# Kernel tuning notes

Measured on AMD Instinct MI355X. Metric: run time of the kernel, lower is better.

## Reference

```python
import jax, jax.numpy as jnp
import numpy as np

N = 100000   # nodes
E = 600000   # edges (before self loops)
D = 128      # dim_latent = H*F
H = 4        # heads
F = 32       # out_feats per head
L = 3        # num GATConv layers (conv_0 + 2)


def setup_inputs() -> dict:
    key = jax.random.key(0)
    ks = jax.random.split(key, 10)
    return {
        "weights": jax.random.normal(ks[0], (N,), jnp.float32),
        "lin_W": jax.random.normal(ks[1], (D, 1), jnp.float32) * 0.1,
        "lin_b": jnp.zeros((D,), jnp.float32),
        "fc_W": jax.random.normal(ks[2], (L, D, D), jnp.float32) * (1.0 / np.sqrt(D)),
        "attn_l": jax.random.normal(ks[3], (L, H, F), jnp.float32) * 0.1,
        "attn_r": jax.random.normal(ks[4], (L, H, F), jnp.float32) * 0.1,
        "conv_b": jnp.zeros((L, D), jnp.float32),
        "pred_W": jax.random.normal(ks[5], (1, D), jnp.float32) * 0.1,
        "pred_b": jnp.zeros((1,), jnp.float32),
        "src": jax.random.randint(ks[6], (E,), 0, N, jnp.int32),
        "dst": jax.random.randint(ks[7], (E,), 0, N, jnp.int32),
    }


def _leaky(x, slope):
    return jnp.where(x >= 0, x, slope * x)


def _gat_conv(x, fc_W, attn_l, attn_r, bias, src, dst):
    # DGL GATConv: bias-free fc, per-head additive attention, edge softmax over dst
    h = (x @ fc_W.T).reshape(N, H, F)                      # [N,H,F]
    el = jnp.sum(h * attn_l[None], axis=-1)                # [N,H]
    er = jnp.sum(h * attn_r[None], axis=-1)                # [N,H]
    e = _leaky(el[src] + er[dst], 0.2)                     # [Etot,H]
    m = jax.ops.segment_max(e, dst, num_segments=N)        # [N,H]
    a = jnp.exp(e - m[dst])                                # [Etot,H]
    s = jax.ops.segment_sum(a, dst, num_segments=N)        # [N,H]
    alpha = a / s[dst]                                     # [Etot,H]
    msg = h[src] * alpha[:, :, None]                       # [Etot,H,F]
    out = jax.ops.segment_sum(msg, dst, num_segments=N)    # [N,H,F]
    out = out + bias.reshape(H, F)[None]
    return out.reshape(N, H * F)


def reference(weights, lin_W, lin_b, fc_W, attn_l, attn_r, conv_b, pred_W, pred_b, src, dst):
    # add self loops (dgl.add_self_loop)
    loop = jnp.arange(N, dtype=src.dtype)
    s_full = jnp.concatenate([src, loop])
    d_full = jnp.concatenate([dst, loop])

    x = weights[:, None] @ lin_W.T + lin_b                 # [N,D]
    for i in range(L):
        if i > 0:
            x = _leaky(x, 0.01)                            # nn.LeakyReLU default
        x = _gat_conv(x, fc_W[i], attn_l[i], attn_r[i], conv_b[i], s_full, d_full)
    logits = x @ pred_W.T + pred_b                         # [N,1]
    return logits
```

## Files before the change

### kernel.cpp

```cpp
#include <hip/hip_runtime.h>
#include <hip/hip_bf16.h>
#include <math.h>


__device__ __forceinline__ float leaky02(float x) {
    return x >= 0.f ? x : 0.2f * x;
}
__device__ __forceinline__ float leaky01(float x) {
    return x >= 0.f ? x : 0.01f * x;
}

__device__ __forceinline__ unsigned short f2bf(float f) {
    unsigned u = __float_as_uint(f);
    unsigned r = u + 0x7FFFu + ((u >> 16) & 1u);
    return (unsigned short)(r >> 16);
}
__device__ __forceinline__ float bf2f(unsigned short s) {
    return __uint_as_float(((unsigned)s) << 16);
}

typedef __attribute__((ext_vector_type(8))) short bf16x8;
typedef __attribute__((ext_vector_type(8))) unsigned short u16x8;
typedef __attribute__((ext_vector_type(4))) float f32x4;

__global__ __launch_bounds__(1024) void prep_kernel(
    int* __restrict__ deg, int N,
    const float* __restrict__ fc_W, const float* __restrict__ attn_l,
    const float* __restrict__ attn_r,
    short* __restrict__ Wh, short* __restrict__ Wl,
    short* __restrict__ Mh, short* __restrict__ Ml,
    const float* __restrict__ lW, const float* __restrict__ lb,
    const float* __restrict__ cb2, const float* __restrict__ pW,
    const float* __restrict__ pb,
    float* __restrict__ c1, float* __restrict__ c2, float* __restrict__ prm,
    int* __restrict__ base_ctr)
{
    const int nbi = (N + 1023) >> 10;
    const int b = blockIdx.x;
    const int t = threadIdx.x;
    if (b == 0 && t == 0) *base_ctr = 0;

    if (b < nbi) {
        int i = b * 1024 + t;
        if (i < N) deg[i] = 1;
        if (i < 2 * 16384) {
            const float* W = fc_W + 16384;
            int l    = i >> 14;
            int p    = i & 16383;
            int j    = p & 7;
            int lane = (p >> 3) & 63;
            int c    = (p >> 9) & 7;
            int kk   = p >> 12;
            int mr   = lane & 15;
            int quad = lane >> 4;
            int row  = c * 16 + mr;
            int d    = kk * 32 + quad * 8 + j;
            float f = W[(size_t)l * 16384 + row * 128 + d];
            unsigned short hi = f2bf(f);
            Wh[i] = (short)hi;
            Wl[i] = (short)f2bf(f - bf2f(hi));
        }
    } else if (b < nbi + 2) {
        int l = b - nbi;
        const float* W  = fc_W + (size_t)(l + 1) * 16384;
        const float* al = attn_l + (l + 1) * 128;
        const float* ar = attn_r + (l + 1) * 128;
        short* mh = Mh + (size_t)l * 16 * 128;
        short* ml = Ml + (size_t)l * 16 * 128;
        int r = t >> 7;
        int d = t & 127;
        int hh = r & 3;
        const float* av = (r < 4) ? al : ar;
        float s = 0.f;
#pragma unroll
        for (int f = 0; f < 32; ++f)
            s += W[(size_t)(hh * 32 + f) * 128 + d] * av[hh * 32 + f];
        unsigned short hi = f2bf(s);
        mh[r * 128 + d] = (short)hi;
        ml[r * 128 + d] = (short)f2bf(s - bf2f(hi));
        mh[(r + 8) * 128 + d] = 0;
        ml[(r + 8) * 128 + d] = 0;
    } else {
        __shared__ float sh1[128], sh2[128], sh3[128], sh4[128], sh5[128];
        const float* W0 = fc_W;
        const float* al = attn_l;
        const float* ar = attn_r;
        int j = t >> 3, sub = t & 7;
        float s1 = 0.f, s2 = 0.f;
        int d0 = sub * 16;
#pragma unroll
        for (int k = 0; k < 16; ++k) {
            float wv = W0[j * 128 + d0 + k];
            s1 += lW[d0 + k] * wv;
            s2 += lb[d0 + k] * wv;
        }
#pragma unroll
        for (int m = 1; m <= 4; m <<= 1) {
            s1 += __shfl_xor(s1, m, 64);
            s2 += __shfl_xor(s2, m, 64);
        }
        if (sub == 0) {
            c1[j] = s1; c2[j] = s2;
            sh1[j] = s1 * al[j]; sh2[j] = s2 * al[j];
            sh3[j] = s1 * ar[j]; sh4[j] = s2 * ar[j];
            sh5[j] = cb2[j] * pW[j];
        }
        __syncthreads();
        if (t < 4) {
            float p = 0.f, q = 0.f, r = 0.f, s = 0.f;
            for (int f = 0; f < 32; ++f) {
                p += sh1[t * 32 + f]; q += sh2[t * 32 + f];
                r += sh3[t * 32 + f]; s += sh4[t * 32 + f];
            }
            prm[t] = p; prm[4 + t] = q; prm[8 + t] = r; prm[12 + t] = s;
        }
        if (t == 0) {
            float cs = 0.f;
            for (int k = 0; k < 128; ++k) cs += sh5[k];
            prm[16] = cs + pb[0];
        }
    }
}

__global__ __launch_bounds__(256) void deg_count_slot_kernel(
    const int* __restrict__ dst, int* __restrict__ deg,
    int* __restrict__ slot, int E)
{
    int i = blockIdx.x * 256 + threadIdx.x;
    if (i < E) slot[i] = atomicAdd(&deg[dst[i]], 1);
}

__global__ __launch_bounds__(1024) void scan_kernel(
    const int* __restrict__ deg, int* __restrict__ base_ctr,
    int* __restrict__ rowp, int* __restrict__ col, int N)
{
    __shared__ int sh[1024];
    __shared__ int sbase;
    int b = blockIdx.x, t = threadIdx.x;
    int i = b * 1024 + t;
    int v = (i < N) ? deg[i] : 0;
    sh[t] = v;
    __syncthreads();
    for (int off = 1; off < 1024; off <<= 1) {
        int u = (t >= off) ? sh[t - off] : 0;
        __syncthreads();
        sh[t] += u;
        __syncthreads();
    }
    if (t == 1023) sbase = atomicAdd(base_ctr, sh[1023]);
    __syncthreads();
    int pre = sbase + sh[t] - v;
    if (i < N) {
        rowp[i] = pre;
        col[pre] = i;
    }
}

__global__ __launch_bounds__(256) void scatter2_kernel(
    const int* __restrict__ src, const int* __restrict__ dst,
    const int* __restrict__ slot, const int* __restrict__ rowp,
    int* __restrict__ col, int E)
{
    int i = blockIdx.x * 256 + threadIdx.x;
    if (i < E) col[rowp[dst[i]] + slot[i]] = src[i];
}

__global__ __launch_bounds__(256) void agg0_kernel(
    const float* __restrict__ w, const float* __restrict__ c1,
    const float* __restrict__ c2, const float* __restrict__ prm,
    const int* __restrict__ rowp, const int* __restrict__ deg,
    const int* __restrict__ col, const float* __restrict__ bias,
    unsigned short* __restrict__ xout, int N)
{
    const int lane = threadIdx.x & 63;
    const int q    = lane >> 4;
    const int l16  = lane & 15;
    const int v    = blockIdx.x * 16 + (threadIdx.x >> 6) * 4 + q;
    if (v >= N) return;

    const int r0 = rowp[v];
    const int r1 = r0 + deg[v];
    const int head = l16 >> 2;
    const int e4   = l16 & 3;
    const int f0   = l16 * 8;
    const float pl = prm[head],     ql = prm[4 + head];
    const float pr = prm[8 + head], qr = prm[12 + head];

    const float wv  = w[v];
    const float erq = wv * pr + qr;
    const float mref = leaky02(wv * pl + ql + erq);

    float S = 0.f, Sw = 0.f;
    for (int j = r0 + e4; j < r1; j += 4) {
        int u = col[j];
        float wu = w[u];
        float e = leaky02(wu * pl + ql + erq);
        float d = fminf(e - mref, 80.f);
        float p = __expf(d);
        S += p; Sw += p * wu;
    }
    S  += __shfl_xor(S, 1, 64);  S  += __shfl_xor(S, 2, 64);
    Sw += __shfl_xor(Sw, 1, 64); Sw += __shfl_xor(Sw, 2, 64);
    const float t = Sw / S;

    float4 a0 = *reinterpret_cast<const float4*>(&c1[f0]);
    float4 a1 = *reinterpret_cast<const float4*>(&c1[f0 + 4]);
    float4 g0 = *reinterpret_cast<const float4*>(&c2[f0]);
    float4 g1 = *reinterpret_cast<const float4*>(&c2[f0 + 4]);
    float4 b0 = *reinterpret_cast<const float4*>(&bias[f0]);
    float4 b1 = *reinterpret_cast<const float4*>(&bias[f0 + 4]);
    const float aa[8] = {a0.x, a0.y, a0.z, a0.w, a1.x, a1.y, a1.z, a1.w};
    const float gg[8] = {g0.x, g0.y, g0.z, g0.w, g1.x, g1.y, g1.z, g1.w};
    const float bb[8] = {b0.x, b0.y, b0.z, b0.w, b1.x, b1.y, b1.z, b1.w};

    u16x8 o;
#pragma unroll
    for (int k = 0; k < 8; ++k)
        o[k] = f2bf(leaky01(t * aa[k] + gg[k] + bb[k]));
    *reinterpret_cast<u16x8*>(&xout[(size_t)v * 128 + f0]) = o;
}

__global__ __launch_bounds__(256) void gemm_mfma_kernel(
    const unsigned short* __restrict__ xb, const short* __restrict__ Wh,
    const short* __restrict__ Wl, const short* __restrict__ Mh,
    const short* __restrict__ Ml, unsigned short* __restrict__ hb,
    float* __restrict__ el, float* __restrict__ er,
    const float* __restrict__ pW, float* __restrict__ yel,
    int N, int mode)
{
    const int lane = threadIdx.x & 63;
    const int wv   = threadIdx.x >> 6;
    const int m0   = blockIdx.x * 128 + wv * 32;
    const int mr   = lane & 15;
    const int quad = lane >> 4;

    int r0 = m0 + mr;      if (r0 > N - 1) r0 = N - 1;
    int r1 = m0 + 16 + mr; if (r1 > N - 1) r1 = N - 1;
    const unsigned short* xp0 = xb + (size_t)r0 * 128 + quad * 8;
    const unsigned short* xp1 = xb + (size_t)r1 * 128 + quad * 8;

    f32x4 acc0[8], acc1[8], acce0, acce1;
#pragma unroll
    for (int c = 0; c < 8; ++c) {
        acc0[c] = (f32x4){0.f, 0.f, 0.f, 0.f};
        acc1[c] = (f32x4){0.f, 0.f, 0.f, 0.f};
    }
    acce0 = (f32x4){0.f, 0.f, 0.f, 0.f};
    acce1 = (f32x4){0.f, 0.f, 0.f, 0.f};

#pragma unroll
    for (int kk = 0; kk < 4; ++kk) {
        bf16x8 a0 = *reinterpret_cast<const bf16x8*>(xp0 + kk * 32);
        bf16x8 a1 = *reinterpret_cast<const bf16x8*>(xp1 + kk * 32);

        const int kb = kk * 32 + quad * 8;
        bf16x8 bh[8], bl[8];
#pragma unroll
        for (int c = 0; c < 8; ++c) {
            const size_t wo = (size_t)((kk * 8 + c) * 64 + lane) * 8;
            bh[c] = *reinterpret_cast<const bf16x8*>(Wh + wo);
            bl[c] = *reinterpret_cast<const bf16x8*>(Wl + wo);
        }
        bf16x8 eh = *reinterpret_cast<const bf16x8*>(Mh + (size_t)mr * 128 + kb);
        bf16x8 eo = *reinterpret_cast<const bf16x8*>(Ml + (size_t)mr * 128 + kb);
#pragma unroll
        for (int c = 0; c < 8; ++c) {
            acc0[c] = __builtin_amdgcn_mfma_f32_16x16x32_bf16(a0, bh[c], acc0[c], 0, 0, 0);
            acc0[c] = __builtin_amdgcn_mfma_f32_16x16x32_bf16(a0, bl[c], acc0[c], 0, 0, 0);
            acc1[c] = __builtin_amdgcn_mfma_f32_16x16x32_bf16(a1, bh[c], acc1[c], 0, 0, 0);
            acc1[c] = __builtin_amdgcn_mfma_f32_16x16x32_bf16(a1, bl[c], acc1[c], 0, 0, 0);
        }
        acce0 = __builtin_amdgcn_mfma_f32_16x16x32_bf16(a0, eh, acce0, 0, 0, 0);
        acce0 = __builtin_amdgcn_mfma_f32_16x16x32_bf16(a0, eo, acce0, 0, 0, 0);
        acce1 = __builtin_amdgcn_mfma_f32_16x16x32_bf16(a1, eh, acce1, 0, 0, 0);
        acce1 = __builtin_amdgcn_mfma_f32_16x16x32_bf16(a1, eo, acce1, 0, 0, 0);
    }

    if (mode == 0) {
#pragma unroll
        for (int i = 0; i < 4; ++i) {
            int rowA = m0 + quad * 4 + i;
            if (rowA < N) {
                unsigned short* hp = hb + (size_t)rowA * 128 + mr;
#pragma unroll
                for (int c = 0; c < 8; ++c) hp[c * 16] = f2bf(acc0[c][i]);
                if (mr < 4)       el[(size_t)rowA * 4 + mr]       = acce0[i];
                else if (mr < 8)  er[(size_t)rowA * 4 + (mr - 4)] = acce0[i];
            }
            int rowB = m0 + 16 + quad * 4 + i;
            if (rowB < N) {
                unsigned short* hp = hb + (size_t)rowB * 128 + mr;
#pragma unroll
                for (int c = 0; c < 8; ++c) hp[c * 16] = f2bf(acc1[c][i]);
                if (mr < 4)       el[(size_t)rowB * 4 + mr]       = acce1[i];
                else if (mr < 8)  er[(size_t)rowB * 4 + (mr - 4)] = acce1[i];
            }
        }
    } else {
        float pw[8];
#pragma unroll
        for (int c = 0; c < 8; ++c) pw[c] = pW[mr + c * 16];
#pragma unroll
        for (int i = 0; i < 4; ++i) {
            int rowA = m0 + quad * 4 + i;
            {
                float y[4];
#pragma unroll
                for (int h = 0; h < 4; ++h)
                    y[h] = acc0[2 * h][i] * pw[2 * h] + acc0[2 * h + 1][i] * pw[2 * h + 1];
#pragma unroll
                for (int d = 1; d < 16; d <<= 1) {
#pragma unroll
                    for (int h = 0; h < 4; ++h) y[h] += __shfl_xor(y[h], d, 64);
                }
                if (rowA < N) {
                    if (mr < 4) {
                        float2 o; o.x = y[mr]; o.y = acce0[i];
                        *reinterpret_cast<float2*>(&yel[(size_t)rowA * 8 + mr * 2]) = o;
                    } else if (mr < 8) {
                        er[(size_t)rowA * 4 + (mr - 4)] = acce0[i];
                    }
                }
            }
            int rowB = m0 + 16 + quad * 4 + i;
            {
                float y[4];
#pragma unroll
                for (int h = 0; h < 4; ++h)
                    y[h] = acc1[2 * h][i] * pw[2 * h] + acc1[2 * h + 1][i] * pw[2 * h + 1];
#pragma unroll
                for (int d = 1; d < 16; d <<= 1) {
#pragma unroll
                    for (int h = 0; h < 4; ++h) y[h] += __shfl_xor(y[h], d, 64);
                }
                if (rowB < N) {
                    if (mr < 4) {
                        float2 o; o.x = y[mr]; o.y = acce1[i];
                        *reinterpret_cast<float2*>(&yel[(size_t)rowB * 8 + mr * 2]) = o;
                    } else if (mr < 8) {
                        er[(size_t)rowB * 4 + (mr - 4)] = acce1[i];
                    }
                }
            }
        }
    }
}

__global__ __launch_bounds__(256) void agg_mid_kernel(
    const unsigned short* __restrict__ hb, const float* __restrict__ el,
    const float* __restrict__ er, const int* __restrict__ rowp,
    const int* __restrict__ deg, const int* __restrict__ col,
    const float* __restrict__ bias, unsigned short* __restrict__ xout, int N)
{
    const int lane = threadIdx.x & 63;
    const int q    = lane >> 4;
    const int l16  = lane & 15;
    const int v    = blockIdx.x * 16 + (threadIdx.x >> 6) * 4 + q;
    if (v >= N) return;

    const int r0 = rowp[v];
    const int r1 = r0 + deg[v];
    const int head = l16 >> 2;
    const int f0   = l16 * 8;
    const float erq = er[(size_t)v * 4 + head];
    const float el_self = el[(size_t)v * 4 + head];
    const float mref = leaky02(el_self + erq);

    float s = 0.f;
    float acc[8];
#pragma unroll
    for (int k = 0; k < 8; ++k) acc[k] = 0.f;

    float elA = el_self;
    u16x8 hvA = *reinterpret_cast<const u16x8*>(&hb[(size_t)v * 128 + f0]);
    int jB = (r0 + 1 < r1) ? r0 + 1 : r1 - 1;
    int uB = col[jB];
    float elB = el[(size_t)uB * 4 + head];
    u16x8 hvB = *reinterpret_cast<const u16x8*>(&hb[(size_t)uB * 128 + f0]);

    for (int j = r0; j < r1; j += 2) {
        int jA2 = (j + 2 < r1) ? j + 2 : r1 - 1;
        int uA2 = col[jA2];
        float elA2 = el[(size_t)uA2 * 4 + head];
        u16x8 hvA2 = *reinterpret_cast<const u16x8*>(&hb[(size_t)uA2 * 128 + f0]);

        {
            float e = leaky02(elA + erq);
            float d = fminf(e - mref, 80.f);
            float p = __expf(d);
            s += p;
#pragma unroll
            for (int k = 0; k < 8; ++k) acc[k] += p * bf2f(hvA[k]);
        }

        if (j + 1 < r1) {
            int jB2 = (j + 3 < r1) ? j + 3 : r1 - 1;
            int uB2 = col[jB2];
            float elB2 = el[(size_t)uB2 * 4 + head];
            u16x8 hvB2 = *reinterpret_cast<const u16x8*>(&hb[(size_t)uB2 * 128 + f0]);

            float e = leaky02(elB + erq);
            float d = fminf(e - mref, 80.f);
            float p = __expf(d);
            s += p;
#pragma unroll
            for (int k = 0; k < 8; ++k) acc[k] += p * bf2f(hvB[k]);

            elB = elB2; hvB = hvB2;
        }
        elA = elA2; hvA = hvA2;
    }
    const float is = 1.f / s;

    float4 b0 = *reinterpret_cast<const float4*>(&bias[f0]);
    float4 b1 = *reinterpret_cast<const float4*>(&bias[f0 + 4]);
    const float bb[8] = {b0.x, b0.y, b0.z, b0.w, b1.x, b1.y, b1.z, b1.w};

    u16x8 o;
#pragma unroll
    for (int k = 0; k < 8; ++k) o[k] = f2bf(leaky01(acc[k] * is + bb[k]));
    *reinterpret_cast<u16x8*>(&xout[(size_t)v * 128 + f0]) = o;
}

__global__ __launch_bounds__(256) void agg2_kernel(
    const float* __restrict__ yel, const float* __restrict__ er,
    const int* __restrict__ rowp, const int* __restrict__ deg,
    const int* __restrict__ col, const float* __restrict__ prm,
    float* __restrict__ logits, int N)
{
    const int lane = threadIdx.x & 63;
    const int q    = lane >> 4;
    const int l16  = lane & 15;
    const int v    = blockIdx.x * 16 + (threadIdx.x >> 6) * 4 + q;
    if (v >= N) return;

    const int r0 = rowp[v];
    const int r1 = r0 + deg[v];
    const int head = l16 >> 2;
    const int e4   = l16 & 3;
    const float erq = er[(size_t)v * 4 + head];

    float2 selfy = *reinterpret_cast<const float2*>(&yel[(size_t)v * 8 + head * 2]);
    const float mref = leaky02(selfy.y + erq);

    float S = 0.f, A = 0.f;
    for (int j = r0 + e4; j < r1; j += 4) {
        int u = col[j];
        float2 c = *reinterpret_cast<const float2*>(&yel[(size_t)u * 8 + head * 2]);
        float e = leaky02(c.y + erq);
        float d = fminf(e - mref, 80.f);
        float p = __expf(d);
        S += p; A += p * c.x;
    }
    S += __shfl_xor(S, 1, 64); S += __shfl_xor(S, 2, 64);
    A += __shfl_xor(A, 1, 64); A += __shfl_xor(A, 2, 64);
    float part = A / S;
    part += __shfl_xor(part, 4, 64);
    part += __shfl_xor(part, 8, 64);
    if (l16 == 0) logits[v] = part + prm[16];
}

extern "C" void kernel_launch(void* const* d_in, const int* in_sizes, int n_in,
                              void* d_out, int out_size, void* d_ws, size_t ws_size,
                              hipStream_t stream)
{
    const float* weights = (const float*)d_in[0];
    const float* lin_W   = (const float*)d_in[1];
    const float* lin_b   = (const float*)d_in[2];
    const float* fc_W    = (const float*)d_in[3];
    const float* attn_l  = (const float*)d_in[4];
    const float* attn_r  = (const float*)d_in[5];
    const float* conv_b  = (const float*)d_in[6];
    const float* pred_W  = (const float*)d_in[7];
    const float* pred_b  = (const float*)d_in[8];
    const int*   src     = (const int*)d_in[9];
    const int*   dst     = (const int*)d_in[10];

    const int N = in_sizes[0];
    const int E = in_sizes[9];
    const int NB1024 = (N + 1023) / 1024;

    unsigned short* xb = (unsigned short*)d_ws;
    unsigned short* hb = xb + (size_t)N * 128;
    float* el  = (float*)(hb + (size_t)N * 128);
    float* er  = el + (size_t)N * 4;
    float* yel = er + (size_t)N * 4;
    float* c1  = yel + (size_t)N * 8;
    float* c2  = c1 + 128;
    float* prm = c2 + 128;
    short* Whs = (short*)(prm + 32);
    short* Wls = Whs + 2 * 16384;
    short* Mhs = Wls + 2 * 16384;
    short* Mls = Mhs + 2 * 2048;
    int*   deg  = (int*)(Mls + 2 * 2048);
    int*   rowp = deg + N;
    int*   slot = rowp + (N + 1);
    int*   col  = slot + E;
    int*   bctr = col + (E + N);

    prep_kernel<<<NB1024 + 3, 1024, 0, stream>>>(
        deg, N, fc_W, attn_l, attn_r, Whs, Wls, Mhs, Mls,
        lin_W, lin_b, conv_b + 2 * 128, pred_W, pred_b, c1, c2, prm, bctr);

    deg_count_slot_kernel<<<(E + 255) / 256, 256, 0, stream>>>(dst, deg, slot, E);

    scan_kernel<<<NB1024, 1024, 0, stream>>>(deg, bctr, rowp, col, N);

    scatter2_kernel<<<(E + 255) / 256, 256, 0, stream>>>(src, dst, slot, rowp, col, E);

    agg0_kernel<<<(N + 15) / 16, 256, 0, stream>>>(
        weights, c1, c2, prm, rowp, deg, col, conv_b, xb, N);

    gemm_mfma_kernel<<<(N + 127) / 128, 256, 0, stream>>>(
        xb, Whs, Wls, Mhs, Mls, hb, el, er, pred_W, yel, N, 0);

    agg_mid_kernel<<<(N + 15) / 16, 256, 0, stream>>>(
        hb, el, er, rowp, deg, col, conv_b + 128, xb, N);

    gemm_mfma_kernel<<<(N + 127) / 128, 256, 0, stream>>>(
        xb, Whs + 16384, Wls + 16384, Mhs + 2048, Mls + 2048,
        hb, el, er, pred_W, yel, N, 1);

    agg2_kernel<<<(N + 15) / 16, 256, 0, stream>>>(
        yel, er, rowp, deg, col, prm, (float*)d_out, N);
}
```

Baseline: 248.5 us.

## Store hidden features in 16-column slabs and split mid aggregation per slab

The first GEMM now writes the bf16 hidden features as eight 16-feature column slabs, with el stored head-major. The middle aggregation kernel launches eight times as many blocks, each gathering one slab with one 2-byte element per lane. The aim is to shrink the random-gather footprint per block and improve cache locality. In exchange, the CSR indices, el lookups and softmax exponentials are repeated for every slab, and each gather becomes a much narrower memory access.

```diff
diff --git a/kernel.cpp b/kernel.cpp
--- a/kernel.cpp
+++ b/kernel.cpp
@@ -281,18 +281,18 @@
         for (int i = 0; i < 4; ++i) {
             int rowA = m0 + quad * 4 + i;
             if (rowA < N) {
-                unsigned short* hp = hb + (size_t)rowA * 128 + mr;
-#pragma unroll
-                for (int c = 0; c < 8; ++c) hp[c * 16] = f2bf(acc0[c][i]);
-                if (mr < 4)       el[(size_t)rowA * 4 + mr]       = acce0[i];
+#pragma unroll
+                for (int c = 0; c < 8; ++c)
+                    hb[((size_t)c * N + rowA) * 16 + mr] = f2bf(acc0[c][i]);
+                if (mr < 4)       el[(size_t)mr * N + rowA]       = acce0[i];
                 else if (mr < 8)  er[(size_t)rowA * 4 + (mr - 4)] = acce0[i];
             }
             int rowB = m0 + 16 + quad * 4 + i;
             if (rowB < N) {
-                unsigned short* hp = hb + (size_t)rowB * 128 + mr;
-#pragma unroll
-                for (int c = 0; c < 8; ++c) hp[c * 16] = f2bf(acc1[c][i]);
-                if (mr < 4)       el[(size_t)rowB * 4 + mr]       = acce1[i];
+#pragma unroll
+                for (int c = 0; c < 8; ++c)
+                    hb[((size_t)c * N + rowB) * 16 + mr] = f2bf(acc1[c][i]);
+                if (mr < 4)       el[(size_t)mr * N + rowB]       = acce1[i];
                 else if (mr < 8)  er[(size_t)rowB * 4 + (mr - 4)] = acce1[i];
             }
         }
@@ -347,79 +347,67 @@
 }
 
 __global__ __launch_bounds__(256) void agg_mid_kernel(
-    const unsigned short* __restrict__ hb, const float* __restrict__ el,
+    const unsigned short* __restrict__ hb_s, const float* __restrict__ el_t,
     const float* __restrict__ er, const int* __restrict__ rowp,
     const int* __restrict__ deg, const int* __restrict__ col,
     const float* __restrict__ bias, unsigned short* __restrict__ xout, int N)
 {
+    const int s    = blockIdx.x & 7;
+    const int bg   = blockIdx.x >> 3;
     const int lane = threadIdx.x & 63;
     const int q    = lane >> 4;
     const int l16  = lane & 15;
-    const int v    = blockIdx.x * 16 + (threadIdx.x >> 6) * 4 + q;
+    const int v    = bg * 16 + (threadIdx.x >> 6) * 4 + q;
     if (v >= N) return;
+
+    const int head = s >> 1;
+    const unsigned short* slab = hb_s + (size_t)s * N * 16;
+    const float* elh = el_t + (size_t)head * N;
 
     const int r0 = rowp[v];
     const int r1 = r0 + deg[v];
-    const int head = l16 >> 2;
-    const int f0   = l16 * 8;
     const float erq = er[(size_t)v * 4 + head];
-    const float el_self = el[(size_t)v * 4 + head];
+    const float el_self = elh[v];
     const float mref = leaky02(el_self + erq);
 
-    float s = 0.f;
-    float acc[8];
-#pragma unroll
-    for (int k = 0; k < 8; ++k) acc[k] = 0.f;
+    float ssum = 0.f, acc = 0.f;
 
     float elA = el_self;
-    u16x8 hvA = *reinterpret_cast<const u16x8*>(&hb[(size_t)v * 128 + f0]);
+    unsigned short hA = slab[(size_t)v * 16 + l16];
     int jB = (r0 + 1 < r1) ? r0 + 1 : r1 - 1;
     int uB = col[jB];
-    float elB = el[(size_t)uB * 4 + head];
-    u16x8 hvB = *reinterpret_cast<const u16x8*>(&hb[(size_t)uB * 128 + f0]);
+    float elB = elh[uB];
+    unsigned short hB = slab[(size_t)uB * 16 + l16];
 
     for (int j = r0; j < r1; j += 2) {
         int jA2 = (j + 2 < r1) ? j + 2 : r1 - 1;
         int uA2 = col[jA2];
-        float elA2 = el[(size_t)uA2 * 4 + head];
-        u16x8 hvA2 = *reinterpret_cast<const u16x8*>(&hb[(size_t)uA2 * 128 + f0]);
+        float elA2 = elh[uA2];
+        unsigned short hA2 = slab[(size_t)uA2 * 16 + l16];
 
         {
             float e = leaky02(elA + erq);
             float d = fminf(e - mref, 80.f);
             float p = __expf(d);
-            s += p;
-#pragma unroll
-            for (int k = 0; k < 8; ++k) acc[k] += p * bf2f(hvA[k]);
-        }
-
+            ssum += p; acc += p * bf2f(hA);
+        }
         if (j + 1 < r1) {
             int jB2 = (j + 3 < r1) ? j + 3 : r1 - 1;
             int uB2 = col[jB2];
-            float elB2 = el[(size_t)uB2 * 4 + head];
-            u16x8 hvB2 = *reinterpret_cast<const u16x8*>(&hb[(size_t)uB2 * 128 + f0]);
+            float elB2 = elh[uB2];
+            unsigned short hB2 = slab[(size_t)uB2 * 16 + l16];
 
             float e = leaky02(elB + erq);
             float d = fminf(e - mref, 80.f);
             float p = __expf(d);
-            s += p;
-#pragma unroll
-            for (int k = 0; k < 8; ++k) acc[k] += p * bf2f(hvB[k]);
-
-            elB = elB2; hvB = hvB2;
-        }
-        elA = elA2; hvA = hvA2;
-    }
-    const float is = 1.f / s;
-
-    float4 b0 = *reinterpret_cast<const float4*>(&bias[f0]);
-    float4 b1 = *reinterpret_cast<const float4*>(&bias[f0 + 4]);
-    const float bb[8] = {b0.x, b0.y, b0.z, b0.w, b1.x, b1.y, b1.z, b1.w};
-
-    u16x8 o;
-#pragma unroll
-    for (int k = 0; k < 8; ++k) o[k] = f2bf(leaky01(acc[k] * is + bb[k]));
-    *reinterpret_cast<u16x8*>(&xout[(size_t)v * 128 + f0]) = o;
+            ssum += p; acc += p * bf2f(hB);
+
+            elB = elB2; hB = hB2;
+        }
+        elA = elA2; hA = hA2;
+    }
+    const int f = s * 16 + l16;
+    xout[(size_t)v * 128 + f] = f2bf(leaky01(acc / ssum + bias[f]));
 }
 
 __global__ __launch_bounds__(256) void agg2_kernel(
@@ -514,7 +502,7 @@
     gemm_mfma_kernel<<<(N + 127) / 128, 256, 0, stream>>>(
         xb, Whs, Wls, Mhs, Mls, hb, el, er, pred_W, yel, N, 0);
 
-    agg_mid_kernel<<<(N + 15) / 16, 256, 0, stream>>>(
+    agg_mid_kernel<<<((N + 15) / 16) * 8, 256, 0, stream>>>(
         hb, el, er, rowp, deg, col, conv_b + 128, xb, N);
 
     gemm_mfma_kernel<<<(N + 127) / 128, 256, 0, stream>>>(
```

Result: slower. 373.9 us (+50.4%).
